# Kernel tuning notes

Hardware: AMD Instinct MI355X
Metric: run time of the kernel (lower is better)

## Reference

```python
import jax, jax.numpy as jnp
import numpy as np

B, S, V, E, H, NL, DFF = 16, 16, 64, 64, 8, 4, 2048
L = S * V
DH = E // H
NUM_GRIDS = 100
POI_DIM = 8
OV_DIM = 8


def setup_inputs() -> dict:
    key = jax.random.key(0)
    ks = jax.random.split(key, 32)
    sc = 0.05
    inp = {}
    inp['features'] = jax.random.normal(ks[0], (B, S, V, 3), jnp.float32)
    inp['overlap_tag'] = jax.random.randint(ks[1], (B, S, V), 0, 3)
    inp['poi_id'] = jax.random.randint(ks[2], (B, S, V), 0, NUM_GRIDS + 1)
    # embedders
    inp['W_raw'] = jax.random.normal(ks[3], (3, E), jnp.float32) * sc
    inp['b_raw'] = jnp.zeros((E,), jnp.float32)
    inp['pos_tab'] = jax.random.normal(ks[4], (S, E), jnp.float32) * sc
    inp['type_tab'] = jax.random.normal(ks[5], (V, E), jnp.float32) * sc
    inp['poi_tab'] = jax.random.normal(ks[6], (NUM_GRIDS + 1, POI_DIM), jnp.float32) * sc
    inp['overlap_tab'] = jax.random.normal(ks[7], (3, OV_DIM), jnp.float32) * sc
    inp['W_comb'] = jax.random.normal(ks[8], (E + OV_DIM + POI_DIM, E), jnp.float32) * sc
    inp['b_comb'] = jnp.zeros((E,), jnp.float32)
    # transformer layers (stacked over NL)
    inp['Wqkv'] = jax.random.normal(ks[9], (NL, E, 3 * E), jnp.float32) * sc
    inp['bqkv'] = jnp.zeros((NL, 3 * E), jnp.float32)
    inp['Wo'] = jax.random.normal(ks[10], (NL, E, E), jnp.float32) * sc
    inp['bo'] = jnp.zeros((NL, E), jnp.float32)
    inp['ln1_s'] = jnp.ones((NL, E), jnp.float32)
    inp['ln1_b'] = jnp.zeros((NL, E), jnp.float32)
    inp['W1'] = jax.random.normal(ks[11], (NL, E, DFF), jnp.float32) * sc
    inp['b1'] = jnp.zeros((NL, DFF), jnp.float32)
    inp['W2'] = jax.random.normal(ks[12], (NL, DFF, E), jnp.float32) * sc
    inp['b2'] = jnp.zeros((NL, E), jnp.float32)
    inp['ln2_s'] = jnp.ones((NL, E), jnp.float32)
    inp['ln2_b'] = jnp.zeros((NL, E), jnp.float32)
    inp['W_head'] = jax.random.normal(ks[13], (E, 3), jnp.float32) * sc
    inp['b_head'] = jnp.zeros((3,), jnp.float32)
    return inp


def _layer_norm(x, s, b):
    m = x.mean(-1, keepdims=True)
    v = ((x - m) ** 2).mean(-1, keepdims=True)
    return (x - m) / jnp.sqrt(v + 1e-5) * s + b


def _forward(features, overlap_tag, poi_id, W_raw, b_raw, pos_tab, type_tab,
             poi_tab, overlap_tab, W_comb, b_comb, Wqkv, bqkv, Wo, bo,
             ln1_s, ln1_b, W1, b1, W2, b2, ln2_s, ln2_b, W_head, b_head):
    # padding_idx=0 rows are zero (as in nn.Embedding(padding_idx=0))
    poi_tab = poi_tab.at[0].set(0.0)
    overlap_tab = overlap_tab.at[0].set(0.0)

    zero_mask = (features.sum(-1) == 0).reshape(B, L)  # [B, L]
    ov_idx = jnp.maximum(overlap_tag, 0)
    poi_idx = jnp.maximum(poi_id, 0)

    feat_e = features @ W_raw + b_raw                    # [B,S,V,E]
    concat = jnp.concatenate([feat_e, overlap_tab[ov_idx], poi_tab[poi_idx]], axis=-1)
    x = (concat @ W_comb + b_comb).reshape(B, L, E)      # [B,L,E]

    t_idx = jnp.repeat(jnp.arange(S), V)                 # [L]
    v_idx = jnp.tile(jnp.arange(V), S)                   # [L]
    struct_mask = (t_idx[:, None] != t_idx[None, :]) & (v_idx[:, None] != v_idx[None, :])
    full_mask = struct_mask[None] | zero_mask[:, None, :] | zero_mask[:, :, None]  # [B,L,L]
    bias = jnp.where(full_mask, -jnp.inf, 0.0)[:, None, :, :]  # [B,1,L,L]

    x = x + pos_tab[t_idx][None] + type_tab[v_idx][None]

    scale = 1.0 / jnp.sqrt(jnp.asarray(DH, x.dtype))
    for l in range(NL):
        qkv = x @ Wqkv[l] + bqkv[l]                      # [B,L,3E]
        q, k, v = jnp.split(qkv, 3, axis=-1)
        q = q.reshape(B, L, H, DH)
        k = k.reshape(B, L, H, DH)
        v = v.reshape(B, L, H, DH)
        scores = jnp.einsum('bqhd,bkhd->bhqk', q, k) * scale + bias
        attn = jax.nn.softmax(scores, axis=-1)
        o = jnp.einsum('bhqk,bkhd->bqhd', attn, v).reshape(B, L, E)
        x = _layer_norm(x + o @ Wo[l] + bo[l], ln1_s[l], ln1_b[l])
        ff = jax.nn.relu(x @ W1[l] + b1[l]) @ W2[l] + b2[l]
        x = _layer_norm(x + ff, ln2_s[l], ln2_b[l])

    last = x.reshape(B, S, V, E)[:, -1]                  # [B,V,E]
    return last @ W_head + b_head                        # [B,V,3]


def reference(features, overlap_tag, poi_id, W_raw, b_raw, pos_tab, type_tab,
              poi_tab, overlap_tab, W_comb, b_comb, Wqkv, bqkv, Wo, bo,
              ln1_s, ln1_b, W1, b1, W2, b2, ln2_s, ln2_b, W_head, b_head):
    return _forward(features, overlap_tag, poi_id, W_raw, b_raw, pos_tab, type_tab,
                    poi_tab, overlap_tab, W_comb, b_comb, Wqkv, bqkv, Wo, bo,
                    ln1_s, ln1_b, W1, b1, W2, b2, ln2_s, ln2_b, W_head, b_head)
```

## Files before the change

kernel.cpp:

```cpp
#include <hip/hip_runtime.h>
#include <math.h>

#define BB 16
#define SS 16
#define VVV 64
#define EE 64
#define HHH 8
#define NLAYER 4
#define DFF_ 2048
#define LL 1024
#define BL 16384
#define PERL 131072

typedef __attribute__((ext_vector_type(8))) _Float16 half8;
typedef __attribute__((ext_vector_type(4))) _Float16 half4v;
typedef __attribute__((ext_vector_type(2))) _Float16 half2v;
typedef __attribute__((ext_vector_type(4))) float f32x4;

#if defined(__has_builtin)
#if __has_builtin(__builtin_amdgcn_fdot2)
#define HAVE_FDOT2 1
#endif
#endif

#define SW64(m, k)  (((m) << 6) + ((((k) >> 3) ^ ((m) & 7)) << 3) + ((k) & 7))


__global__ __launch_bounds__(256) void k_prep(
    const float* __restrict__ W1, const float* __restrict__ W2,
    const float* __restrict__ Wqkv, const float* __restrict__ Wo,
    const float* __restrict__ Wcomb,
    _Float16* __restrict__ w1f, _Float16* __restrict__ w2f,
    _Float16* __restrict__ wqkvf, _Float16* __restrict__ wof,
    _Float16* __restrict__ wcombt)
{
  __shared__ float t[64 * 65];
  int bx = blockIdx.x;
  int cc = threadIdx.x & 63, rr = threadIdx.x >> 6;

  if (bx >= 272) {
    int r0 = (bx - 272) * 64;
#pragma unroll
    for (int i = 0; i < 16; i++) {
      int r = i * 4 + rr;
      if (r0 + r < 80) t[r * 65 + cc] = Wcomb[(size_t)(r0 + r) * 64 + cc];
    }
    __syncthreads();
#pragma unroll
    for (int i = 0; i < 16; i++) {
      int c = i * 4 + rr;
      if (r0 + c < 80) wcombt[(size_t)cc * 80 + r0 + c] = (_Float16)t[c * 65 + cc];
    }
    return;
  }

  const float* src; _Float16* dst; int astr;
  if (bx < 128) {
    int l = bx >> 5, g = bx & 31;
    src = W1 + (size_t)l * PERL + g * 64; astr = 2048;
    dst = w1f + (size_t)(l * 32 + g) * 4096;
  } else if (bx < 256) {
    int j = bx - 128; int l = j >> 5, g = j & 31;
    src = W2 + (size_t)l * PERL + (size_t)g * 64 * 64; astr = 64;
    dst = w2f + (size_t)(l * 32 + g) * 4096;
  } else if (bx < 268) {
    int j = bx - 256; int l = j / 3, g = j % 3;
    src = Wqkv + (size_t)l * 64 * 192 + g * 64; astr = 192;
    dst = wqkvf + (size_t)(l * 3 + g) * 4096;
  } else {
    int l = bx - 268;
    src = Wo + (size_t)l * 4096; astr = 64;
    dst = wof + (size_t)l * 4096;
  }
#pragma unroll
  for (int i = 0; i < 16; i++) {
    int a = i * 4 + rr;
    t[cc * 65 + a] = src[(size_t)a * astr + cc];
  }
  __syncthreads();
#pragma unroll
  for (int it = 0; it < 2; it++) {
    int c = threadIdx.x + it * 256;
    int frag = c >> 6, lane = c & 63;
    int m = (frag >> 1) * 16 + (lane & 15);
    int k0 = (frag & 1) * 32 + (lane >> 4) * 8;
    const float* tr = &t[m * 65 + k0];
    half8 h;
#pragma unroll
    for (int j = 0; j < 8; j++) h[j] = (_Float16)tr[j];
    *(half8*)&dst[(size_t)c * 8] = h;
  }
}

__device__ __forceinline__ void qkv_nb(
    const half8 (&af)[2][2], const _Float16* __restrict__ wqkvf,
    const float* __restrict__ bqkv, _Float16* __restrict__ qbuf,
    _Float16* __restrict__ kbuf, _Float16* __restrict__ vbuf,
    int bx, int nb, int wm, int wn, int lane)
{
  int quad = lane >> 4, l15 = lane & 15;
  const _Float16* bt = wqkvf + (size_t)nb * 4096;
  half8 bf[2][2];
#pragma unroll
  for (int nt = 0; nt < 2; nt++)
#pragma unroll
    for (int ks = 0; ks < 2; ks++)
      bf[nt][ks] = *(const half8*)&bt[(size_t)(((wn * 2 + nt) * 2 + ks) * 512) +
                                      lane * 8];
  f32x4 acc[2][2];
#pragma unroll
  for (int mt = 0; mt < 2; mt++)
#pragma unroll
    for (int nt = 0; nt < 2; nt++) {
      float bv = bqkv[nb * 64 + wn * 32 + nt * 16 + l15];
      acc[mt][nt] = (f32x4){bv, bv, bv, bv};
    }
#pragma unroll
  for (int ks = 0; ks < 2; ks++)
#pragma unroll
    for (int mt = 0; mt < 2; mt++)
#pragma unroll
      for (int nt = 0; nt < 2; nt++)
        acc[mt][nt] = __builtin_amdgcn_mfma_f32_16x16x32_f16(
            af[mt][ks], bf[nt][ks], acc[mt][nt], 0, 0, 0);
  _Float16* dst = (nb == 0) ? qbuf : ((nb == 1) ? kbuf : vbuf);
#pragma unroll
  for (int mt = 0; mt < 2; mt++)
#pragma unroll
    for (int nt = 0; nt < 2; nt++) {
      int col = wn * 32 + nt * 16 + l15;
      int h = col >> 3, d = col & 7;
#pragma unroll
      for (int r = 0; r < 4; r++) {
        int row = bx * 64 + wm * 32 + mt * 16 + quad * 4 + r;
        int b = row >> 10, rb = row & 1023;
        dst[((size_t)(b * 8 + h) * 1024 + rb) * 8 + d] = (_Float16)acc[mt][nt][r];
      }
    }
}

__device__ __forceinline__ void ffn_load2(
    const _Float16* __restrict__ w1f, const _Float16* __restrict__ w2f, int g,
    half8 (&a1)[2][2], half8 (&b2w)[2][2], int wn, int lane)
{
  const _Float16* w1t_ = w1f + (size_t)g * 4096;
  const _Float16* w2t_ = w2f + (size_t)g * 4096;
#pragma unroll
  for (int ht = 0; ht < 2; ht++)
#pragma unroll
    for (int ks = 0; ks < 2; ks++)
      a1[ht][ks] = *(const half8*)&w1t_[(size_t)(((wn * 2 + ht) * 2 + ks) * 512) +
                                        lane * 8];
#pragma unroll
  for (int nt = 0; nt < 2; nt++)
#pragma unroll
    for (int ks = 0; ks < 2; ks++)
      b2w[nt][ks] = *(const half8*)&w2t_[(size_t)(((wn * 2 + nt) * 2 + ks) * 512) +
                                         lane * 8];
}

__device__ __forceinline__ void ffn_step2(
    const half8 (&a1)[2][2], const half8 (&b2w)[2][2], const half8 (&xb)[2][2],
    _Float16* hsbuf, const float* __restrict__ b1, int g, f32x4 (&acc)[2][2],
    int wn, int lane)
{
  int quad = lane >> 4, l15 = lane & 15;
  f32x4 hacc[2][2];
#pragma unroll
  for (int ht = 0; ht < 2; ht++)
#pragma unroll
    for (int mt = 0; mt < 2; mt++) hacc[ht][mt] = (f32x4){0.f, 0.f, 0.f, 0.f};
#pragma unroll
  for (int ks = 0; ks < 2; ks++)
#pragma unroll
    for (int ht = 0; ht < 2; ht++)
#pragma unroll
      for (int mt = 0; mt < 2; mt++)
        hacc[ht][mt] = __builtin_amdgcn_mfma_f32_16x16x32_f16(
            a1[ht][ks], xb[mt][ks], hacc[ht][mt], 0, 0, 0);
#pragma unroll
  for (int ht = 0; ht < 2; ht++) {
    float4 bb = *(const float4*)&b1[g * 64 + wn * 32 + ht * 16 + quad * 4];
#pragma unroll
    for (int mt = 0; mt < 2; mt++) {
      f32x4 hv = hacc[ht][mt];
      half4v hp = (half4v){
          (_Float16)fmaxf(hv[0] + bb.x, 0.f), (_Float16)fmaxf(hv[1] + bb.y, 0.f),
          (_Float16)fmaxf(hv[2] + bb.z, 0.f), (_Float16)fmaxf(hv[3] + bb.w, 0.f)};
      *(half4v*)&hsbuf[SW64(mt * 16 + l15, wn * 32 + ht * 16 + quad * 4)] = hp;
    }
  }
  __syncthreads();
#pragma unroll
  for (int ks = 0; ks < 2; ks++)
#pragma unroll
    for (int mt = 0; mt < 2; mt++) {
      half8 a2 = *(const half8*)&hsbuf[SW64(mt * 16 + l15, ks * 32 + quad * 8)];
#pragma unroll
      for (int nt = 0; nt < 2; nt++)
        acc[mt][nt] = __builtin_amdgcn_mfma_f32_16x16x32_f16(a2, b2w[nt][ks],
                                                             acc[mt][nt], 0, 0, 0);
    }
}

__global__ __launch_bounds__(256) void k_embqkv(
    const float* __restrict__ features, const int* __restrict__ ovtag,
    const int* __restrict__ poiid, const float* __restrict__ W_raw,
    const float* __restrict__ b_raw, const float* __restrict__ ov_tab,
    const float* __restrict__ poi_tab, const _Float16* __restrict__ wcombt,
    const float* __restrict__ b_comb, const float* __restrict__ pos_tab,
    const float* __restrict__ type_tab, float* __restrict__ x1,
    float* __restrict__ zm, const _Float16* __restrict__ wqkvf,
    const float* __restrict__ bqkv, _Float16* __restrict__ qbuf,
    _Float16* __restrict__ kbuf, _Float16* __restrict__ vbuf)
{
  constexpr int KP = 104;
  __shared__ _Float16 As[64 * KP];
  __shared__ _Float16 Bs[64 * KP];
  __shared__ _Float16 xs[4096];
  int tid = threadIdx.x;
  int bx = blockIdx.x;
  int m0 = bx * 64;
  int wave = tid >> 6, lane = tid & 63, quad = lane >> 4, l15 = lane & 15;
  int wm = wave >> 1, wn = wave & 1;
  for (int p = tid; p < 1536; p += 256) {
    int r = p / 24, s = p - r * 24; int c = s * 4;
    int row = m0 + r;
    float f0 = features[row * 3 + 0];
    float f1 = features[row * 3 + 1];
    float f2 = features[row * 3 + 2];
    if (s == 0) zm[row] = ((f0 + f1 + f2) == 0.f) ? 1.f : 0.f;
    half4v h;
#pragma unroll
    for (int j = 0; j < 4; j++) {
      int cc = c + j; float v;
      if (cc < 64) {
        v = b_raw[cc] + f0 * W_raw[cc] + f1 * W_raw[64 + cc] + f2 * W_raw[128 + cc];
      } else if (cc < 72) {
        int tt = ovtag[row]; v = (tt <= 0) ? 0.f : ov_tab[tt * 8 + cc - 64];
      } else if (cc < 80) {
        int tt = poiid[row]; v = (tt <= 0) ? 0.f : poi_tab[tt * 8 + cc - 72];
      } else v = 0.f;
      h[j] = (_Float16)v;
    }
    *(half4v*)&As[r * KP + c] = h;
  }
  for (int p = tid; p < 1536; p += 256) {
    int r = p / 24, s = p - r * 24; int c = s * 4;
    half4v h = (half4v){0, 0, 0, 0};
    if (c < 80) h = *(const half4v*)&wcombt[r * 80 + c];
    *(half4v*)&Bs[r * KP + c] = h;
  }
  __syncthreads();
  f32x4 acc[2][2];
#pragma unroll
  for (int mt = 0; mt < 2; mt++)
#pragma unroll
    for (int nt = 0; nt < 2; nt++) {
      float bv = b_comb[wn * 32 + nt * 16 + l15];
      acc[mt][nt] = (f32x4){bv, bv, bv, bv};
    }
#pragma unroll
  for (int ks = 0; ks < 3; ks++) {
    half8 af[2], bf[2];
#pragma unroll
    for (int mt = 0; mt < 2; mt++)
      af[mt] = *(const half8*)&As[(wm * 32 + mt * 16 + l15) * KP + ks * 32 + quad * 8];
#pragma unroll
    for (int nt = 0; nt < 2; nt++)
      bf[nt] = *(const half8*)&Bs[(wn * 32 + nt * 16 + l15) * KP + ks * 32 + quad * 8];
#pragma unroll
    for (int mt = 0; mt < 2; mt++)
#pragma unroll
      for (int nt = 0; nt < 2; nt++)
        acc[mt][nt] = __builtin_amdgcn_mfma_f32_16x16x32_f16(af[mt], bf[nt],
                                                             acc[mt][nt], 0, 0, 0);
  }
#pragma unroll
  for (int mt = 0; mt < 2; mt++)
#pragma unroll
    for (int nt = 0; nt < 2; nt++)
#pragma unroll
      for (int r = 0; r < 4; r++) {
        int lrow = wm * 32 + mt * 16 + quad * 4 + r;
        int row = m0 + lrow;
        int col = wn * 32 + nt * 16 + l15;
        int l = row & (LL - 1);
        float v = acc[mt][nt][r] +
            pos_tab[(l >> 6) * 64 + col] + type_tab[(l & 63) * 64 + col];
        x1[(size_t)row * 64 + col] = v;
        xs[SW64(lrow, col)] = (_Float16)v;
      }
  __syncthreads();
  half8 af[2][2];
#pragma unroll
  for (int mt = 0; mt < 2; mt++)
#pragma unroll
    for (int ks = 0; ks < 2; ks++)
      af[mt][ks] = *(const half8*)&xs[SW64(wm * 32 + mt * 16 + l15,
                                           ks * 32 + quad * 8)];
  for (int nb = 0; nb < 3; nb++)
    qkv_nb(af, wqkvf, bqkv, qbuf, kbuf, vbuf, bx, nb, wm, wn, lane);
}

__global__ __launch_bounds__(256, 2) void k_layerf(
    const _Float16* __restrict__ qin, const _Float16* __restrict__ kin,
    const _Float16* __restrict__ vin, const float* __restrict__ zm,
    const _Float16* __restrict__ wof, const float* __restrict__ bo,
    float* __restrict__ x1,
    const float* __restrict__ ln1_s, const float* __restrict__ ln1_b,
    const _Float16* __restrict__ w1f, const _Float16* __restrict__ w2f,
    const float* __restrict__ b1, const float* __restrict__ b2,
    const float* __restrict__ ln2_s, const float* __restrict__ ln2_b,
    const _Float16* __restrict__ wqkvf, const float* __restrict__ bqkv,
    _Float16* __restrict__ qout, _Float16* __restrict__ kout,
    _Float16* __restrict__ vout, int doqkv,
    const float* __restrict__ Wh, const float* __restrict__ bh,
    float* __restrict__ out)
{
  __shared__ float ots[32 * 68];
  __shared__ __align__(16) _Float16 xs[2048];
  __shared__ float x2f[2048];
  __shared__ __align__(16) _Float16 hs[2][2][2048];
  __shared__ __align__(16) _Float16 os[2048];
  __shared__ float zsh[1024];
  int tid = threadIdx.x;
  int bx = blockIdx.x;
  int r0 = bx * 32;
  int wave = tid >> 6, lane = tid & 63;
  int quad = lane >> 4, l15 = lane & 15;
  int grp = wave >> 1, wn = wave & 1;
  int b = r0 >> 10;

  for (int p = tid; p < 1024; p += 256) zsh[p] = zm[b * LL + p];
  __syncthreads();

  {
    int lr = tid & 31, hh = tid >> 5;
    int rb = (r0 & 1023) + lr;
    int tq = rb >> 6, vq = rb & 63;
    const _Float16* kb = kin + (size_t)(b * 8 + hh) * 8192;
    const _Float16* vb = vin + (size_t)(b * 8 + hh) * 8192;
    half8 qh = *(const half8*)&qin[(size_t)(b * 8 + hh) * 8192 + (size_t)rb * 8];
    const float scale = 0.3535533905932738f;
    float m = -INFINITY, lsum = 0.f;
    float acc[8] = {0.f, 0.f, 0.f, 0.f, 0.f, 0.f, 0.f, 0.f};
    bool zmq = (zsh[rb] != 0.f);

    auto attend = [&](int k) {
      if (zsh[k] != 0.f) return;
      half8 kk = *(const half8*)&kb[(size_t)k * 8];
      float s = 0.f;
#ifdef HAVE_FDOT2
#pragma unroll
      for (int j = 0; j < 4; j++) {
        half2v qa = (half2v){qh[2 * j], qh[2 * j + 1]};
        half2v ka = (half2v){kk[2 * j], kk[2 * j + 1]};
        s = __builtin_amdgcn_fdot2(qa, ka, s, false);
      }
#else
#pragma unroll
      for (int j = 0; j < 8; j++) s += (float)qh[j] * (float)kk[j];
#endif
      s *= scale;
      half8 vv = *(const half8*)&vb[(size_t)k * 8];
      float nm = fmaxf(m, s);
      float r = __expf(m - nm);
      float p = __expf(s - nm);
      lsum = lsum * r + p;
#pragma unroll
      for (int d = 0; d < 8; d++) acc[d] = acc[d] * r + p * (float)vv[d];
      m = nm;
    };

    if (!zmq) {
      for (int vv2 = 0; vv2 < 64; vv2++) attend(tq * 64 + vv2);
      for (int tt = 0; tt < 16; tt++) {
        if (tt == tq) continue;
        attend(tt * 64 + vq);
      }
    }
    float inv = 1.f / lsum;
    half8 o;
#pragma unroll
    for (int d = 0; d < 8; d++) o[d] = (_Float16)(acc[d] * inv);
    *(half8*)&os[SW64(lr, hh * 8)] = o;
  }
  __syncthreads();

  {
    half8 af[2], bf[2][2];
#pragma unroll
    for (int ks = 0; ks < 2; ks++)
      af[ks] = *(const half8*)&os[SW64(grp * 16 + l15, ks * 32 + quad * 8)];
#pragma unroll
    for (int nt = 0; nt < 2; nt++)
#pragma unroll
      for (int ks = 0; ks < 2; ks++)
        bf[nt][ks] = *(const half8*)&wof[(size_t)(((wn * 2 + nt) * 2 + ks) * 512) +
                                         lane * 8];
    f32x4 acc[2];
#pragma unroll
    for (int nt = 0; nt < 2; nt++) {
      float bv = bo[wn * 32 + nt * 16 + l15];
      acc[nt] = (f32x4){bv, bv, bv, bv};
    }
#pragma unroll
    for (int ks = 0; ks < 2; ks++)
#pragma unroll
      for (int nt = 0; nt < 2; nt++)
        acc[nt] = __builtin_amdgcn_mfma_f32_16x16x32_f16(af[ks], bf[nt][ks],
                                                         acc[nt], 0, 0, 0);
#pragma unroll
    for (int nt = 0; nt < 2; nt++)
#pragma unroll
      for (int r = 0; r < 4; r++)
        ots[(grp * 16 + quad * 4 + r) * 68 + wn * 32 + nt * 16 + l15] = acc[nt][r];
  }
  __syncthreads();
  for (int i = 0; i < 8; i++) {
    int row = wave * 8 + i;
    size_t off = (size_t)(r0 + row) * 64 + lane;
    float val = ots[row * 68 + lane] + x1[off];
    float sum = val;
#pragma unroll
    for (int o = 32; o > 0; o >>= 1) sum += __shfl_xor(sum, o);
    float mean = sum * (1.f / 64.f);
    float d = val - mean;
    float sq = d * d;
#pragma unroll
    for (int o = 32; o > 0; o >>= 1) sq += __shfl_xor(sq, o);
    float xv = d * rsqrtf(sq * (1.f / 64.f) + 1e-5f) * ln1_s[lane] + ln1_b[lane];
    x2f[row * 64 + lane] = xv;
    xs[SW64(row, lane)] = (_Float16)xv;
  }
  __syncthreads();

  half8 xb[2][2];
#pragma unroll
  for (int mt = 0; mt < 2; mt++)
#pragma unroll
    for (int ks = 0; ks < 2; ks++)
      xb[mt][ks] = *(const half8*)&xs[SW64(mt * 16 + l15, ks * 32 + quad * 8)];
  f32x4 acc[2][2];
#pragma unroll
  for (int mt = 0; mt < 2; mt++)
#pragma unroll
    for (int nt = 0; nt < 2; nt++) {
      float bv = (grp == 0) ? b2[wn * 32 + nt * 16 + l15] : 0.f;
      acc[mt][nt] = (f32x4){bv, bv, bv, bv};
    }
  half8 a1x[2][2], b2x[2][2], a1y[2][2], b2y[2][2];
  ffn_load2(w1f, w2f, grp, a1x, b2x, wn, lane);
  for (int ii = 0; ii < 8; ii++) {
    ffn_load2(w1f, w2f, ii * 4 + 2 + grp, a1y, b2y, wn, lane);
    ffn_step2(a1x, b2x, xb, &hs[grp][0][0], b1, ii * 4 + grp, acc, wn, lane);
    if (ii < 7) ffn_load2(w1f, w2f, ii * 4 + 4 + grp, a1x, b2x, wn, lane);
    ffn_step2(a1y, b2y, xb, &hs[grp][1][0], b1, ii * 4 + 2 + grp, acc, wn, lane);
  }
  __syncthreads();
  if (grp == 0) {
#pragma unroll
    for (int mt = 0; mt < 2; mt++)
#pragma unroll
      for (int nt = 0; nt < 2; nt++)
#pragma unroll
        for (int r = 0; r < 4; r++)
          ots[(mt * 16 + quad * 4 + r) * 68 + wn * 32 + nt * 16 + l15] =
              acc[mt][nt][r];
  }
  __syncthreads();
  if (grp == 1) {
#pragma unroll
    for (int mt = 0; mt < 2; mt++)
#pragma unroll
      for (int nt = 0; nt < 2; nt++)
#pragma unroll
        for (int r = 0; r < 4; r++)
          ots[(mt * 16 + quad * 4 + r) * 68 + wn * 32 + nt * 16 + l15] +=
              acc[mt][nt][r];
  }
  __syncthreads();
  for (int i = 0; i < 8; i++) {
    int row = wave * 8 + i;
    size_t off = (size_t)(r0 + row) * 64 + lane;
    float val = ots[row * 68 + lane] + x2f[row * 64 + lane];
    float sum = val;
#pragma unroll
    for (int o = 32; o > 0; o >>= 1) sum += __shfl_xor(sum, o);
    float mean = sum * (1.f / 64.f);
    float d = val - mean;
    float sq = d * d;
#pragma unroll
    for (int o = 32; o > 0; o >>= 1) sq += __shfl_xor(sq, o);
    float xv = d * rsqrtf(sq * (1.f / 64.f) + 1e-5f) * ln2_s[lane] + ln2_b[lane];
    x1[off] = xv;
    x2f[row * 64 + lane] = xv;
    xs[SW64(row, lane)] = (_Float16)xv;
  }
  if (!doqkv) {
    __syncthreads();
    if ((bx & 31) >= 30 && tid < 96) {
      int bb2 = bx >> 5;
      int i = tid / 3, j = tid - i * 3;
      int vglob = (bx & 1) * 32 + i;
      float a = bh[j];
      for (int e = 0; e < 64; e++)
        a += x2f[i * 64 + e] * Wh[e * 3 + j];
      out[((size_t)(bb2 * 64 + vglob)) * 3 + j] = a;
    }
    return;
  }
  __syncthreads();
  half8 af[2][2];
#pragma unroll
  for (int mt = 0; mt < 2; mt++)
#pragma unroll
    for (int ks = 0; ks < 2; ks++)
      af[mt][ks] = *(const half8*)&xs[SW64(mt * 16 + l15, ks * 32 + quad * 8)];
  for (int nb = 0; nb < 3; nb++) {
    const _Float16* bt = wqkvf + (size_t)nb * 4096;
    half8 bf[2];
#pragma unroll
    for (int ks = 0; ks < 2; ks++)
      bf[ks] = *(const half8*)&bt[(size_t)((wave * 2 + ks) * 512) + lane * 8];
    f32x4 qacc[2];
#pragma unroll
    for (int mt = 0; mt < 2; mt++) {
      float bv = bqkv[nb * 64 + wave * 16 + l15];
      qacc[mt] = (f32x4){bv, bv, bv, bv};
    }
#pragma unroll
    for (int ks = 0; ks < 2; ks++)
#pragma unroll
      for (int mt = 0; mt < 2; mt++)
        qacc[mt] = __builtin_amdgcn_mfma_f32_16x16x32_f16(af[mt][ks], bf[ks],
                                                          qacc[mt], 0, 0, 0);
    _Float16* dst = (nb == 0) ? qout : ((nb == 1) ? kout : vout);
    int col = wave * 16 + l15;
    int h2 = col >> 3, d2 = col & 7;
#pragma unroll
    for (int mt = 0; mt < 2; mt++)
#pragma unroll
      for (int r = 0; r < 4; r++) {
        int row = r0 + mt * 16 + quad * 4 + r;
        int rbq = row & 1023;
        dst[((size_t)(b * 8 + h2) * 1024 + rbq) * 8 + d2] = (_Float16)qacc[mt][r];
      }
  }
}

extern "C" void kernel_launch(void* const* d_in, const int* in_sizes, int n_in,
                              void* d_out, int out_size, void* d_ws, size_t ws_size,
                              hipStream_t stream) {
  const float* features = (const float*)d_in[0];
  const int*   ovtag    = (const int*)d_in[1];
  const int*   poiid    = (const int*)d_in[2];
  const float* W_raw    = (const float*)d_in[3];
  const float* b_raw    = (const float*)d_in[4];
  const float* pos_tab  = (const float*)d_in[5];
  const float* type_tab = (const float*)d_in[6];
  const float* poi_tab  = (const float*)d_in[7];
  const float* ov_tab   = (const float*)d_in[8];
  const float* W_comb   = (const float*)d_in[9];
  const float* b_comb   = (const float*)d_in[10];
  const float* Wqkv     = (const float*)d_in[11];
  const float* bqkv     = (const float*)d_in[12];
  const float* Wo       = (const float*)d_in[13];
  const float* bo       = (const float*)d_in[14];
  const float* ln1_s    = (const float*)d_in[15];
  const float* ln1_b    = (const float*)d_in[16];
  const float* W1       = (const float*)d_in[17];
  const float* b1       = (const float*)d_in[18];
  const float* W2       = (const float*)d_in[19];
  const float* b2       = (const float*)d_in[20];
  const float* ln2_s    = (const float*)d_in[21];
  const float* ln2_b    = (const float*)d_in[22];
  const float* W_head   = (const float*)d_in[23];
  const float* b_head   = (const float*)d_in[24];
  float* out = (float*)d_out;
  float* ws  = (float*)d_ws;

  float* zm  = ws;
  float* x1  = zm + BL;
  _Float16* qbA = (_Float16*)(x1 + (size_t)BL * 64);
  _Float16* kbA = qbA + (size_t)BL * 64;
  _Float16* vbA = kbA + (size_t)BL * 64;
  _Float16* qbB = vbA + (size_t)BL * 64;
  _Float16* kbB = qbB + (size_t)BL * 64;
  _Float16* vbB = kbB + (size_t)BL * 64;
  _Float16* wcombt = vbB + (size_t)BL * 64;
  _Float16* w1f    = wcombt + 5120;
  _Float16* w2f    = w1f + (size_t)NLAYER * PERL;
  _Float16* wqkvf  = w2f + (size_t)NLAYER * PERL;
  _Float16* wof    = wqkvf + (size_t)NLAYER * 3 * 4096;

  k_prep<<<274, 256, 0, stream>>>(W1, W2, Wqkv, Wo, W_comb,
                                  w1f, w2f, wqkvf, wof, wcombt);
  k_embqkv<<<256, 256, 0, stream>>>(features, ovtag, poiid, W_raw, b_raw,
                                    ov_tab, poi_tab, wcombt, b_comb,
                                    pos_tab, type_tab, x1, zm,
                                    wqkvf, bqkv, qbA, kbA, vbA);
  for (int l = 0; l < NLAYER; l++) {
    const _Float16* qin = (l & 1) ? qbB : qbA;
    const _Float16* kin = (l & 1) ? kbB : kbA;
    const _Float16* vin = (l & 1) ? vbB : vbA;
    _Float16* qout = (l & 1) ? qbA : qbB;
    _Float16* kout = (l & 1) ? kbA : kbB;
    _Float16* vout = (l & 1) ? vbA : vbB;
    int doqkv = (l < NLAYER - 1);
    k_layerf<<<512, 256, 0, stream>>>(
        qin, kin, vin, zm,
        wof + (size_t)l * 4096, bo + l * EE, x1,
        ln1_s + l * EE, ln1_b + l * EE,
        w1f + (size_t)l * PERL, w2f + (size_t)l * PERL,
        b1 + l * DFF_, b2 + l * EE,
        ln2_s + l * EE, ln2_b + l * EE,
        wqkvf + (size_t)(l + 1 < NLAYER ? l + 1 : 0) * 3 * 4096,
        bqkv + (l + 1 < NLAYER ? l + 1 : 0) * 192,
        qout, kout, vout, doqkv, W_head, b_head, out);
  }
}
```

Measured before the change: 310.1 us.

## Give each wave its own FFN chunks to drop per-step barriers, branchless masked attention

The FFN loop is restructured so each of the four waves owns whole 64-wide hidden chunks and its own LDS scratch. This removes the block-wide __syncthreads inside every FFN step, and the four partial results are reduced through two shared buffers. Attention masking becomes an additive -20000 bias instead of a per-key branch. Wo fragments, the residual x1 values and the LN and bias parameters are prefetched into registers before the attention phase. Register pressure rises a lot (four sets of 4x2 weight fragments plus 2x4 accumulators), which may cut occupancy under launch_bounds(256,2), and masked keys are now fully computed rather than skipped.

```diff
diff --git a/kernel.cpp b/kernel.cpp
--- a/kernel.cpp
+++ b/kernel.cpp
@@ -139,66 +139,54 @@
     }
 }
 
-__device__ __forceinline__ void ffn_load2(
-    const _Float16* __restrict__ w1f, const _Float16* __restrict__ w2f, int g,
-    half8 (&a1)[2][2], half8 (&b2w)[2][2], int wn, int lane)
+__device__ __forceinline__ void ffn_loadw(const _Float16* __restrict__ wt,
+                                          half8 (&fr)[4][2], int lane)
 {
-  const _Float16* w1t_ = w1f + (size_t)g * 4096;
-  const _Float16* w2t_ = w2f + (size_t)g * 4096;
-#pragma unroll
-  for (int ht = 0; ht < 2; ht++)
-#pragma unroll
-    for (int ks = 0; ks < 2; ks++)
-      a1[ht][ks] = *(const half8*)&w1t_[(size_t)(((wn * 2 + ht) * 2 + ks) * 512) +
-                                        lane * 8];
-#pragma unroll
-  for (int nt = 0; nt < 2; nt++)
-#pragma unroll
-    for (int ks = 0; ks < 2; ks++)
-      b2w[nt][ks] = *(const half8*)&w2t_[(size_t)(((wn * 2 + nt) * 2 + ks) * 512) +
-                                         lane * 8];
+#pragma unroll
+  for (int t = 0; t < 4; t++)
+#pragma unroll
+    for (int ks = 0; ks < 2; ks++)
+      fr[t][ks] = *(const half8*)&wt[(size_t)((t * 2 + ks) * 512) + lane * 8];
 }
 
-__device__ __forceinline__ void ffn_step2(
-    const half8 (&a1)[2][2], const half8 (&b2w)[2][2], const half8 (&xb)[2][2],
-    _Float16* hsbuf, const float* __restrict__ b1, int g, f32x4 (&acc)[2][2],
-    int wn, int lane)
+__device__ __forceinline__ void ffn_chunk(
+    const half8 (&a1)[4][2], const half8 (&wb2)[4][2], const half8 (&xb)[2][2],
+    _Float16* hw, const float* __restrict__ b1, int g, f32x4 (&acc)[2][4],
+    int quad, int l15)
 {
-  int quad = lane >> 4, l15 = lane & 15;
-  f32x4 hacc[2][2];
-#pragma unroll
-  for (int ht = 0; ht < 2; ht++)
+  f32x4 hacc[4][2];
+#pragma unroll
+  for (int ht = 0; ht < 4; ht++)
 #pragma unroll
     for (int mt = 0; mt < 2; mt++) hacc[ht][mt] = (f32x4){0.f, 0.f, 0.f, 0.f};
 #pragma unroll
   for (int ks = 0; ks < 2; ks++)
 #pragma unroll
-    for (int ht = 0; ht < 2; ht++)
+    for (int ht = 0; ht < 4; ht++)
 #pragma unroll
       for (int mt = 0; mt < 2; mt++)
         hacc[ht][mt] = __builtin_amdgcn_mfma_f32_16x16x32_f16(
             a1[ht][ks], xb[mt][ks], hacc[ht][mt], 0, 0, 0);
 #pragma unroll
-  for (int ht = 0; ht < 2; ht++) {
-    float4 bb = *(const float4*)&b1[g * 64 + wn * 32 + ht * 16 + quad * 4];
+  for (int ht = 0; ht < 4; ht++) {
+    float4 bb = *(const float4*)&b1[g * 64 + ht * 16 + quad * 4];
 #pragma unroll
     for (int mt = 0; mt < 2; mt++) {
       f32x4 hv = hacc[ht][mt];
       half4v hp = (half4v){
           (_Float16)fmaxf(hv[0] + bb.x, 0.f), (_Float16)fmaxf(hv[1] + bb.y, 0.f),
           (_Float16)fmaxf(hv[2] + bb.z, 0.f), (_Float16)fmaxf(hv[3] + bb.w, 0.f)};
-      *(half4v*)&hsbuf[SW64(mt * 16 + l15, wn * 32 + ht * 16 + quad * 4)] = hp;
-    }
-  }
-  __syncthreads();
+      *(half4v*)&hw[SW64(mt * 16 + l15, ht * 16 + quad * 4)] = hp;
+    }
+  }
 #pragma unroll
   for (int ks = 0; ks < 2; ks++)
 #pragma unroll
     for (int mt = 0; mt < 2; mt++) {
-      half8 a2 = *(const half8*)&hsbuf[SW64(mt * 16 + l15, ks * 32 + quad * 8)];
-#pragma unroll
-      for (int nt = 0; nt < 2; nt++)
-        acc[mt][nt] = __builtin_amdgcn_mfma_f32_16x16x32_f16(a2, b2w[nt][ks],
+      half8 a2 = *(const half8*)&hw[SW64(mt * 16 + l15, ks * 32 + quad * 8)];
+#pragma unroll
+      for (int nt = 0; nt < 4; nt++)
+        acc[mt][nt] = __builtin_amdgcn_mfma_f32_16x16x32_f16(a2, wb2[nt][ks],
                                                              acc[mt][nt], 0, 0, 0);
     }
 }
@@ -319,9 +307,10 @@
     float* __restrict__ out)
 {
   __shared__ float ots[32 * 68];
+  __shared__ float ots2[32 * 68];
   __shared__ __align__(16) _Float16 xs[2048];
   __shared__ float x2f[2048];
-  __shared__ __align__(16) _Float16 hs[2][2][2048];
+  __shared__ __align__(16) _Float16 hs[4][2048];
   __shared__ __align__(16) _Float16 os[2048];
   __shared__ float zsh[1024];
   int tid = threadIdx.x;
@@ -332,7 +321,23 @@
   int grp = wave >> 1, wn = wave & 1;
   int b = r0 >> 10;
 
-  for (int p = tid; p < 1024; p += 256) zsh[p] = zm[b * LL + p];
+  for (int p = tid; p < 1024; p += 256)
+    zsh[p] = (zm[b * LL + p] != 0.f) ? -20000.f : 0.f;
+
+  half8 obf[2][2];
+#pragma unroll
+  for (int nt = 0; nt < 2; nt++)
+#pragma unroll
+    for (int ks = 0; ks < 2; ks++)
+      obf[nt][ks] = *(const half8*)&wof[(size_t)(((wn * 2 + nt) * 2 + ks) * 512) +
+                                        lane * 8];
+  float x1pre[8];
+#pragma unroll
+  for (int i = 0; i < 8; i++)
+    x1pre[i] = x1[(size_t)(r0 + wave * 8 + i) * 64 + lane];
+  float ln1sv = ln1_s[lane], ln1bv = ln1_b[lane];
+  float ln2sv = ln2_s[lane], ln2bv = ln2_b[lane];
+  float fb2 = b2[lane];
   __syncthreads();
 
   {
@@ -343,13 +348,13 @@
     const _Float16* vb = vin + (size_t)(b * 8 + hh) * 8192;
     half8 qh = *(const half8*)&qin[(size_t)(b * 8 + hh) * 8192 + (size_t)rb * 8];
     const float scale = 0.3535533905932738f;
-    float m = -INFINITY, lsum = 0.f;
+    float m = -10000.f, lsum = 0.f;
     float acc[8] = {0.f, 0.f, 0.f, 0.f, 0.f, 0.f, 0.f, 0.f};
-    bool zmq = (zsh[rb] != 0.f);
+    bool zmq = (zsh[rb] < -1.f);
 
     auto attend = [&](int k) {
-      if (zsh[k] != 0.f) return;
       half8 kk = *(const half8*)&kb[(size_t)k * 8];
+      half8 vv = *(const half8*)&vb[(size_t)k * 8];
       float s = 0.f;
 #ifdef HAVE_FDOT2
 #pragma unroll
@@ -362,8 +367,7 @@
 #pragma unroll
       for (int j = 0; j < 8; j++) s += (float)qh[j] * (float)kk[j];
 #endif
-      s *= scale;
-      half8 vv = *(const half8*)&vb[(size_t)k * 8];
+      s = s * scale + zsh[k];
       float nm = fmaxf(m, s);
       float r = __expf(m - nm);
       float p = __expf(s - nm);
@@ -380,7 +384,7 @@
         attend(tt * 64 + vq);
       }
     }
-    float inv = 1.f / lsum;
+    float inv = (lsum > 0.f) ? 1.f / lsum : 0.f;
     half8 o;
 #pragma unroll
     for (int d = 0; d < 8; d++) o[d] = (_Float16)(acc[d] * inv);
@@ -389,16 +393,10 @@
   __syncthreads();
 
   {
-    half8 af[2], bf[2][2];
+    half8 af[2];
 #pragma unroll
     for (int ks = 0; ks < 2; ks++)
       af[ks] = *(const half8*)&os[SW64(grp * 16 + l15, ks * 32 + quad * 8)];
-#pragma unroll
-    for (int nt = 0; nt < 2; nt++)
-#pragma unroll
-      for (int ks = 0; ks < 2; ks++)
-        bf[nt][ks] = *(const half8*)&wof[(size_t)(((wn * 2 + nt) * 2 + ks) * 512) +
-                                         lane * 8];
     f32x4 acc[2];
 #pragma unroll
     for (int nt = 0; nt < 2; nt++) {
@@ -409,7 +407,7 @@
     for (int ks = 0; ks < 2; ks++)
 #pragma unroll
       for (int nt = 0; nt < 2; nt++)
-        acc[nt] = __builtin_amdgcn_mfma_f32_16x16x32_f16(af[ks], bf[nt][ks],
+        acc[nt] = __builtin_amdgcn_mfma_f32_16x16x32_f16(af[ks], obf[nt][ks],
                                                          acc[nt], 0, 0, 0);
 #pragma unroll
     for (int nt = 0; nt < 2; nt++)
@@ -417,11 +415,13 @@
       for (int r = 0; r < 4; r++)
         ots[(grp * 16 + quad * 4 + r) * 68 + wn * 32 + nt * 16 + l15] = acc[nt][r];
   }
+  half8 a1x[4][2], b2x[4][2], a1y[4][2], b2y[4][2];
+  ffn_loadw(w1f + (size_t)wave * 4096, a1x, lane);
+  ffn_loadw(w2f + (size_t)wave * 4096, b2x, lane);
   __syncthreads();
   for (int i = 0; i < 8; i++) {
     int row = wave * 8 + i;
-    size_t off = (size_t)(r0 + row) * 64 + lane;
-    float val = ots[row * 68 + lane] + x1[off];
+    float val = ots[row * 68 + lane] + x1pre[i];
     float sum = val;
 #pragma unroll
     for (int o = 32; o > 0; o >>= 1) sum += __shfl_xor(sum, o);
@@ -430,7 +430,7 @@
     float sq = d * d;
 #pragma unroll
     for (int o = 32; o > 0; o >>= 1) sq += __shfl_xor(sq, o);
-    float xv = d * rsqrtf(sq * (1.f / 64.f) + 1e-5f) * ln1_s[lane] + ln1_b[lane];
+    float xv = d * rsqrtf(sq * (1.f / 64.f) + 1e-5f) * ln1sv + ln1bv;
     x2f[row * 64 + lane] = xv;
     xs[SW64(row, lane)] = (_Float16)xv;
   }
@@ -442,49 +442,50 @@
 #pragma unroll
     for (int ks = 0; ks < 2; ks++)
       xb[mt][ks] = *(const half8*)&xs[SW64(mt * 16 + l15, ks * 32 + quad * 8)];
-  f32x4 acc[2][2];
-#pragma unroll
-  for (int mt = 0; mt < 2; mt++)
-#pragma unroll
-    for (int nt = 0; nt < 2; nt++) {
-      float bv = (grp == 0) ? b2[wn * 32 + nt * 16 + l15] : 0.f;
-      acc[mt][nt] = (f32x4){bv, bv, bv, bv};
-    }
-  half8 a1x[2][2], b2x[2][2], a1y[2][2], b2y[2][2];
-  ffn_load2(w1f, w2f, grp, a1x, b2x, wn, lane);
-  for (int ii = 0; ii < 8; ii++) {
-    ffn_load2(w1f, w2f, ii * 4 + 2 + grp, a1y, b2y, wn, lane);
-    ffn_step2(a1x, b2x, xb, &hs[grp][0][0], b1, ii * 4 + grp, acc, wn, lane);
-    if (ii < 7) ffn_load2(w1f, w2f, ii * 4 + 4 + grp, a1x, b2x, wn, lane);
-    ffn_step2(a1y, b2y, xb, &hs[grp][1][0], b1, ii * 4 + 2 + grp, acc, wn, lane);
-  }
-  __syncthreads();
-  if (grp == 0) {
+  f32x4 facc[2][4];
+#pragma unroll
+  for (int mt = 0; mt < 2; mt++)
+#pragma unroll
+    for (int nt = 0; nt < 4; nt++) facc[mt][nt] = (f32x4){0.f, 0.f, 0.f, 0.f};
+  _Float16* hw = &hs[wave][0];
+  for (int ii = 0; ii < 4; ii++) {
+    int gy = ii * 8 + 4 + wave;
+    ffn_loadw(w1f + (size_t)gy * 4096, a1y, lane);
+    ffn_loadw(w2f + (size_t)gy * 4096, b2y, lane);
+    ffn_chunk(a1x, b2x, xb, hw, b1, ii * 8 + wave, facc, quad, l15);
+    if (ii < 3) {
+      ffn_loadw(w1f + (size_t)(gy + 4) * 4096, a1x, lane);
+      ffn_loadw(w2f + (size_t)(gy + 4) * 4096, b2x, lane);
+    }
+    ffn_chunk(a1y, b2y, xb, hw, b1, gy, facc, quad, l15);
+  }
+  if (wave < 2) {
+    float* dst = (wave == 0) ? ots : ots2;
 #pragma unroll
     for (int mt = 0; mt < 2; mt++)
 #pragma unroll
-      for (int nt = 0; nt < 2; nt++)
+      for (int nt = 0; nt < 4; nt++)
 #pragma unroll
         for (int r = 0; r < 4; r++)
-          ots[(mt * 16 + quad * 4 + r) * 68 + wn * 32 + nt * 16 + l15] =
-              acc[mt][nt][r];
-  }
-  __syncthreads();
-  if (grp == 1) {
+          dst[(mt * 16 + quad * 4 + r) * 68 + nt * 16 + l15] = facc[mt][nt][r];
+  }
+  __syncthreads();
+  if (wave >= 2) {
+    float* dst = (wave == 2) ? ots : ots2;
 #pragma unroll
     for (int mt = 0; mt < 2; mt++)
 #pragma unroll
-      for (int nt = 0; nt < 2; nt++)
+      for (int nt = 0; nt < 4; nt++)
 #pragma unroll
         for (int r = 0; r < 4; r++)
-          ots[(mt * 16 + quad * 4 + r) * 68 + wn * 32 + nt * 16 + l15] +=
-              acc[mt][nt][r];
+          dst[(mt * 16 + quad * 4 + r) * 68 + nt * 16 + l15] += facc[mt][nt][r];
   }
   __syncthreads();
   for (int i = 0; i < 8; i++) {
     int row = wave * 8 + i;
     size_t off = (size_t)(r0 + row) * 64 + lane;
-    float val = ots[row * 68 + lane] + x2f[row * 64 + lane];
+    float val = ots[row * 68 + lane] + ots2[row * 68 + lane] + fb2 +
+                x2f[row * 64 + lane];
     float sum = val;
 #pragma unroll
     for (int o = 32; o > 0; o >>= 1) sum += __shfl_xor(sum, o);
@@ -493,7 +494,7 @@
     float sq = d * d;
 #pragma unroll
     for (int o = 32; o > 0; o >>= 1) sq += __shfl_xor(sq, o);
-    float xv = d * rsqrtf(sq * (1.f / 64.f) + 1e-5f) * ln2_s[lane] + ln2_b[lane];
+    float xv = d * rsqrtf(sq * (1.f / 64.f) + 1e-5f) * ln2sv + ln2bv;
     x1[off] = xv;
     x2f[row * 64 + lane] = xv;
     xs[SW64(row, lane)] = (_Float16)xv;
```

Measured after the change: 291.4 us. -6.0%, faster.
